# Kernel optimization log

Hardware: AMD Instinct MI355X
Metric: run time of the kernel (lower is better)

Reference implementation:

```python
import jax, jax.numpy as jnp
import numpy as np

B, T, X_DIM, H_DIM, C_NUM = 64, 1380, 96, 192, 345
SCALE = 1.0 / (X_DIM ** 0.5 * H_DIM ** 0.5)


def setup_inputs() -> dict:
    key = jax.random.key(0)
    k1, k2, k3, k4 = jax.random.split(key, 4)
    X = jax.random.normal(k1, (B, T, X_DIM), dtype=jnp.float32)
    H = jax.random.normal(k2, (B, T, H_DIM), dtype=jnp.float32)
    W1 = jax.random.normal(k3, (X_DIM, H_DIM), dtype=jnp.float32)
    W2 = jax.random.normal(k4, (C_NUM, T), dtype=jnp.float32)
    return {"X": X, "H": H, "W1": W1, "W2": W2}


def reference(X, H, W1, W2):
    # X: [B,T,x_dim] -> project to h_dim
    Xp = jnp.einsum('btx,xh->bth', X, W1)                 # [B,T,h]
    # batch_dot(X, H, axes=[2,2]) / sqrt(x_dim*h_dim)
    A = jnp.einsum('bth,buh->btu', Xp, H) * SCALE         # [B,T,T]
    # K.dot(W2, A) -> [c,B,T], then permute (1,0,2) -> [B,c,T]
    A = jnp.einsum('ct,btu->bcu', W2, A)                  # [B,c,T]
    A = jax.nn.softmax(A, axis=-1)
    # batch_dot(A, H, axes=[2,1])
    C = jnp.einsum('bcu,buh->bch', A, H)                  # [B,c,h]
    return C
```

## Files before the change

### kernel.cpp

```cpp
#include <hip/hip_runtime.h>
#include <math.h>

namespace {
constexpr int B_  = 64;
constexpr int T_  = 1380;
constexpr int XD_ = 96;
constexpr int HD_ = 192;
constexpr int CN_ = 345;
constexpr int CP_ = 384;
constexpr int TP_ = 1392;
constexpr int TP2_ = 1408;
constexpr int TH_ = 690;
constexpr float SCALE_ = 0.00736569563735987f;
}

typedef __attribute__((ext_vector_type(8))) short bf16x8;
typedef __attribute__((ext_vector_type(4))) float f32x4;
typedef unsigned short u16;
typedef unsigned int   u32;

__device__ __forceinline__ u16 f2bf(float f) {
    union { float f; u32 u; } c; c.f = f;
    u32 r = (c.u + 0x7fffu + ((c.u >> 16) & 1u)) >> 16;
    return (u16)r;
}
__device__ __forceinline__ float bf2f(u16 s) {
    union { u32 u; float f; } c; c.u = ((u32)s) << 16;
    return c.f;
}

__device__ __forceinline__ float red16_max(float v) {
    int ti;
    ti = __builtin_amdgcn_update_dpp(0, __builtin_bit_cast(int, v), 0x128, 0xf, 0xf, true);
    v = fmaxf(v, __builtin_bit_cast(float, ti));
    ti = __builtin_amdgcn_update_dpp(0, __builtin_bit_cast(int, v), 0x124, 0xf, 0xf, true);
    v = fmaxf(v, __builtin_bit_cast(float, ti));
    ti = __builtin_amdgcn_update_dpp(0, __builtin_bit_cast(int, v), 0x122, 0xf, 0xf, true);
    v = fmaxf(v, __builtin_bit_cast(float, ti));
    ti = __builtin_amdgcn_update_dpp(0, __builtin_bit_cast(int, v), 0x121, 0xf, 0xf, true);
    v = fmaxf(v, __builtin_bit_cast(float, ti));
    return v;
}
__device__ __forceinline__ float red16_sum(float v) {
    int ti;
    ti = __builtin_amdgcn_update_dpp(0, __builtin_bit_cast(int, v), 0x128, 0xf, 0xf, true);
    v += __builtin_bit_cast(float, ti);
    ti = __builtin_amdgcn_update_dpp(0, __builtin_bit_cast(int, v), 0x124, 0xf, 0xf, true);
    v += __builtin_bit_cast(float, ti);
    ti = __builtin_amdgcn_update_dpp(0, __builtin_bit_cast(int, v), 0x122, 0xf, 0xf, true);
    v += __builtin_bit_cast(float, ti);
    ti = __builtin_amdgcn_update_dpp(0, __builtin_bit_cast(int, v), 0x121, 0xf, 0xf, true);
    v += __builtin_bit_cast(float, ti);
    return v;
}

__global__ __launch_bounds__(256) void k0_all(const float* __restrict__ Hg,
                                              u16* __restrict__ Hh,
                                              u16* __restrict__ Hl,
                                              u16* __restrict__ Hth,
                                              const float* __restrict__ Xg,
                                              u16* __restrict__ Xth,
                                              u16* __restrict__ Xtl,
                                              const float* __restrict__ W2g,
                                              u16* __restrict__ W2h,
                                              u16* __restrict__ W2l,
                                              const float* __restrict__ W1g,
                                              u16* __restrict__ W1th,
                                              u16* __restrict__ W1tl) {
    __shared__ __align__(16) u16 sb[2][96][72];
    const int tid = threadIdx.x;
    const int L = blockIdx.x;

    if (L < 4224) {
        const int bx = L % 22, by = (L / 22) % 3, b = L / 66;
        const int u0 = bx * 64, h0 = by * 64;
        u16 (*til)[72] = sb[0];
#pragma unroll
        for (int i = 0; i < 2; i++) {
            int task = i * 256 + tid;
            int r = task >> 3;
            int g = task & 7;
            int u = u0 + r;
            float4 va = make_float4(0.f, 0.f, 0.f, 0.f), vb = va;
            if (u < T_) {
                const float* p = Hg + ((size_t)b * T_ + u) * HD_ + h0 + g * 8;
                va = *(const float4*)p;
                vb = *(const float4*)(p + 4);
            }
            float f[8] = {va.x, va.y, va.z, va.w, vb.x, vb.y, vb.z, vb.w};
            u16 hi[8], lo[8];
#pragma unroll
            for (int k = 0; k < 8; k++) {
                hi[k] = f2bf(f[k]);
                lo[k] = f2bf(f[k] - bf2f(hi[k]));
            }
            if (u < T_) {
                size_t base = ((size_t)b * T_ + u) * HD_ + h0 + g * 8;
                *(uint4*)(Hh + base) = *(const uint4*)hi;
                *(uint4*)(Hl + base) = *(const uint4*)lo;
            }
            const int rs = r ^ (g * 8);
#pragma unroll
            for (int k = 0; k < 8; k++) til[g * 8 + k][rs] = hi[k];
        }
        __syncthreads();
#pragma unroll
        for (int i = 0; i < 2; i++) {
            int task = i * 256 + tid;
            int hh = task >> 3;
            int ug = task & 7;
            int q  = ug ^ (hh >> 3);
            int ub = u0 + ug * 8;
            uint4 v = *(const uint4*)&til[hh][q * 8];
            u16* dst = Hth + ((size_t)b * HD_ + h0 + hh) * TP_ + ub;
            if (ub + 8 <= T_) {
                *(uint4*)dst = v;
            } else if (ub < TP_) {
                const u16* pv = (const u16*)&v;
#pragma unroll
                for (int k = 0; k < 8; k++)
                    if (ub + k < TP_) dst[k] = (ub + k < T_) ? pv[k] : (u16)0;
            }
        }
    } else if (L < 5632) {
        const int j = L - 4224;
        const int t0 = (j % 22) * 64, b = j / 22;
        u16 (*tih)[72] = sb[0];
        u16 (*tlo)[72] = sb[1];
#pragma unroll
        for (int i = 0; i < 6; i++) {
            int task = i * 256 + tid;
            int r = task / 24, xg = task % 24;
            float4 v = make_float4(0.f, 0.f, 0.f, 0.f);
            if (t0 + r < T_)
                v = *(const float4*)(Xg + ((size_t)b * T_ + t0 + r) * XD_ + xg * 4);
            float f[4] = {v.x, v.y, v.z, v.w};
            const int rs = r ^ (((xg >> 1) & 7) * 8);
#pragma unroll
            for (int k = 0; k < 4; k++) {
                u16 hi = f2bf(f[k]);
                tih[xg * 4 + k][rs] = hi;
                tlo[xg * 4 + k][rs] = f2bf(f[k] - bf2f(hi));
            }
        }
        __syncthreads();
#pragma unroll
        for (int i = 0; i < 6; i++) {
            int id = i * 256 + tid;
            int buf = (id >= 768);
            int cid = buf ? id - 768 : id;
            int x = cid >> 3, col = cid & 7;
            int q = col ^ ((x >> 3) & 7);
            uint4 v = *(const uint4*)&(buf ? tlo : tih)[x][q * 8];
            u16* dst = (buf ? Xtl : Xth) + ((size_t)b * XD_ + x) * TP2_ + t0 + col * 8;
            *(uint4*)dst = v;
        }
    } else {
        const int j = L - 5632;
        const int i = j * 256 + tid;
        const int n2 = CP_ * (TP2_ / 2);
        if (i < n2) {
            int c = i / (TP2_ / 2), tc = i % (TP2_ / 2);
            int t = tc * 2;
            float v0 = 0.f, v1 = 0.f;
            if (c < CN_) {
                if (t < T_)     v0 = W2g[(size_t)c * T_ + t];
                if (t + 1 < T_) v1 = W2g[(size_t)c * T_ + t + 1];
            }
            u16 h0 = f2bf(v0), h1 = f2bf(v1);
            u16 l0 = f2bf(v0 - bf2f(h0)), l1 = f2bf(v1 - bf2f(h1));
            ((u32*)W2h)[i] = (u32)h0 | ((u32)h1 << 16);
            ((u32*)W2l)[i] = (u32)l0 | ((u32)l1 << 16);
        } else {
            int i1 = i - n2;
            int h = i1 / XD_, x = i1 % XD_;
            float v = W1g[(size_t)x * HD_ + h];
            u16 hi = f2bf(v);
            W1th[i1] = hi;
            W1tl[i1] = f2bf(v - bf2f(hi));
        }
    }
}

__global__ __launch_bounds__(256, 1) void k12_mfma(const u16* __restrict__ W2h,
                                                   const u16* __restrict__ W2l,
                                                   const u16* __restrict__ Xth,
                                                   const u16* __restrict__ Xtl,
                                                   const u16* __restrict__ W1th,
                                                   const u16* __restrict__ W1tl,
                                                   u32* __restrict__ Ysi) {
    __shared__ __align__(16) u16 smem[49152];
    float* sZ = (float*)smem;

    const int tid  = threadIdx.x;
    const int lane = tid & 63;
    const int w    = tid >> 6;
    const int tx   = lane & 15;
    const int quad = lane >> 4;
    const int wr   = w >> 1;
    const int wc2  = w & 1;
    const int L    = blockIdx.x;
    const int xcd  = L & 7;
    const int slot = L >> 3;
    const int b    = xcd * 8 + (slot >> 2);
    const int c0   = (slot & 3) * 96;

    const u16* gsrc;
    size_t rowstart;
    if (w == 0)      { gsrc = W2h; rowstart = (size_t)c0; }
    else if (w == 1) { gsrc = W2l; rowstart = (size_t)c0; }
    else if (w == 2) { gsrc = Xth; rowstart = (size_t)b * XD_; }
    else             { gsrc = Xtl; rowstart = (size_t)b * XD_; }
    const int jg = (lane & 7) ^ ((lane >> 3) & 7);

#define STAGE(bufsel, kk)                                                         \
    {                                                                             \
        u16* lb = smem + (bufsel) * 24576 + w * 6144;                             \
        _Pragma("unroll")                                                         \
        for (int i_ = 0; i_ < 12; i_++) {                                         \
            int row_ = i_ * 8 + (lane >> 3);                                      \
            const u16* gp_ = gsrc + (rowstart + row_) * TP2_ + (kk) + jg * 8;     \
            __builtin_amdgcn_global_load_lds(                                     \
                (const __attribute__((address_space(1))) u32*)(const void*)gp_,   \
                (__attribute__((address_space(3))) u32*)(void*)(lb + i_ * 512),   \
                16, 0, 0);                                                        \
        }                                                                         \
    }

    f32x4 accZ[3][3];
#pragma unroll
    for (int i = 0; i < 3; i++)
#pragma unroll
        for (int j = 0; j < 3; j++) accZ[i][j] = (f32x4){0.f, 0.f, 0.f, 0.f};

    STAGE(0, 0);
    for (int s = 0; s < 22; s++) {
        __builtin_amdgcn_sched_barrier(0);
        if (s < 21) {
            STAGE((s + 1) & 1, (s + 1) * 64);
            asm volatile("s_waitcnt vmcnt(12)" ::: "memory");
        } else {
            asm volatile("s_waitcnt vmcnt(0)" ::: "memory");
        }
        __builtin_amdgcn_s_barrier();
        __builtin_amdgcn_sched_barrier(0);
        const u16* bufp = smem + (s & 1) * 24576;
#pragma unroll
        for (int ks2 = 0; ks2 < 2; ks2++) {
            const int G = ks2 * 4 + quad;
            bf16x8 ah[3], al[3], bh3[3], bl3[3];
#pragma unroll
            for (int am = 0; am < 3; am++) {
                int row = wr * 48 + am * 16 + tx;
                int off = row * 64 + (G ^ (row & 7)) * 8;
                ah[am] = *(const bf16x8*)(bufp + off);
                al[am] = *(const bf16x8*)(bufp + 6144 + off);
            }
#pragma unroll
            for (int bn = 0; bn < 3; bn++) {
                int row = wc2 * 48 + bn * 16 + tx;
                int off = row * 64 + (G ^ (row & 7)) * 8;
                bh3[bn] = *(const bf16x8*)(bufp + 12288 + off);
                bl3[bn] = *(const bf16x8*)(bufp + 18432 + off);
            }
#pragma unroll
            for (int am = 0; am < 3; am++)
#pragma unroll
                for (int bn = 0; bn < 3; bn++) {
                    accZ[am][bn] = __builtin_amdgcn_mfma_f32_16x16x32_bf16(ah[am], bh3[bn], accZ[am][bn], 0, 0, 0);
                    accZ[am][bn] = __builtin_amdgcn_mfma_f32_16x16x32_bf16(ah[am], bl3[bn], accZ[am][bn], 0, 0, 0);
                    accZ[am][bn] = __builtin_amdgcn_mfma_f32_16x16x32_bf16(al[am], bh3[bn], accZ[am][bn], 0, 0, 0);
                }
        }
        asm volatile("s_waitcnt lgkmcnt(0)" ::: "memory");
        __builtin_amdgcn_sched_barrier(0);
        __builtin_amdgcn_s_barrier();
    }
#undef STAGE

    __builtin_amdgcn_sched_barrier(0);
#pragma unroll
    for (int am = 0; am < 3; am++)
#pragma unroll
        for (int bn = 0; bn < 3; bn++)
#pragma unroll
            for (int r = 0; r < 4; r++)
                sZ[(wr * 48 + am * 16 + quad * 4 + r) * 100 + wc2 * 48 + bn * 16 + tx] = accZ[am][bn][r];
    __syncthreads();

    bf16x8 A2h[3][3], A2l[3][3];
#pragma unroll
    for (int am = 0; am < 3; am++)
#pragma unroll
        for (int ks = 0; ks < 3; ks++) {
            const float* zrow = sZ + (wr * 48 + am * 16 + tx) * 100 + ks * 32 + quad * 8;
            bf16x8 vh, vl;
#pragma unroll
            for (int j = 0; j < 8; j++) {
                float v = zrow[j];
                u16 hi = f2bf(v);
                vh[j] = (short)hi;
                vl[j] = (short)f2bf(v - bf2f(hi));
            }
            A2h[am][ks] = vh; A2l[am][ks] = vl;
        }

    f32x4 accY[3][6];
#pragma unroll
    for (int i = 0; i < 3; i++)
#pragma unroll
        for (int j = 0; j < 6; j++) accY[i][j] = (f32x4){0.f, 0.f, 0.f, 0.f};
#pragma unroll
    for (int hn = 0; hn < 6; hn++) {
        const int hrow = wc2 * 96 + hn * 16 + tx;
#pragma unroll
        for (int ks = 0; ks < 3; ks++) {
            bf16x8 bh = *(const bf16x8*)(W1th + (size_t)hrow * XD_ + ks * 32 + quad * 8);
            bf16x8 bl = *(const bf16x8*)(W1tl + (size_t)hrow * XD_ + ks * 32 + quad * 8);
#pragma unroll
            for (int am = 0; am < 3; am++) {
                accY[am][hn] = __builtin_amdgcn_mfma_f32_16x16x32_bf16(A2h[am][ks], bh, accY[am][hn], 0, 0, 0);
                accY[am][hn] = __builtin_amdgcn_mfma_f32_16x16x32_bf16(A2h[am][ks], bl, accY[am][hn], 0, 0, 0);
                accY[am][hn] = __builtin_amdgcn_mfma_f32_16x16x32_bf16(A2l[am][ks], bh, accY[am][hn], 0, 0, 0);
            }
        }
    }

#pragma unroll
    for (int am = 0; am < 3; am++)
#pragma unroll
        for (int r = 0; r < 4; r++) {
            int c = c0 + wr * 48 + am * 16 + quad * 4 + r;
            if (c < CN_) {
                size_t base = ((size_t)b * CN_ + c) * HD_;
#pragma unroll
                for (int hn = 0; hn < 6; hn++) {
                    float y = SCALE_ * accY[am][hn][r];
                    u16 hi = f2bf(y);
                    u16 lo = f2bf(y - bf2f(hi));
                    Ysi[base + wc2 * 96 + hn * 16 + tx] = (u32)hi | ((u32)lo << 16);
                }
            }
        }
}

__global__ __launch_bounds__(768, 3) void k3_mfma(const u32* __restrict__ Ysi,
                                                  const u16* __restrict__ Hh,
                                                  const u16* __restrict__ Hl,
                                                  const u16* __restrict__ Hth,
                                                  float* __restrict__ Op,
                                                  float* __restrict__ Ml,
                                                  float* __restrict__ Ll) {
    __shared__ __align__(16) u16 smem[44544];

    const int tid  = threadIdx.x;
    const int lane = tid & 63;
    const int w    = tid >> 6;
    const int tx   = lane & 15;
    const int quad = lane >> 4;
    const int L    = blockIdx.x;
    const int xcd  = L & 7;
    const int slot = L >> 3;
    const int gp   = xcd * 16 + (slot >> 1);
    const int ct   = slot & 1;
    const int b    = gp >> 1;
    const int sp   = gp & 1;
    const int c0   = ct * 192;
    const int us   = sp * TH_, ue = us + TH_;

    bf16x8 Ah[6], Al[6];
    const int ar = c0 + w * 16 + tx;
    if (ar < CN_) {
        const u32* yi = Ysi + ((size_t)b * CN_ + ar) * HD_;
#pragma unroll
        for (int ks = 0; ks < 6; ks++) {
            u32 vv[8];
            *(uint4*)&vv[0] = *(const uint4*)(yi + ks * 32 + quad * 8);
            *(uint4*)&vv[4] = *(const uint4*)(yi + ks * 32 + quad * 8 + 4);
            bf16x8 hh, ll;
#pragma unroll
            for (int j = 0; j < 8; j++) {
                hh[j] = (short)(vv[j] & 0xffffu);
                ll[j] = (short)(vv[j] >> 16);
            }
            Ah[ks] = hh; Al[ks] = ll;
        }
    } else {
#pragma unroll
        for (int ks = 0; ks < 6; ks++) { Ah[ks] = (bf16x8)0; Al[ks] = (bf16x8)0; }
    }

    float m_s[4], l_s[4];
    f32x4 accO[12];
#pragma unroll
    for (int r = 0; r < 4; r++) { m_s[r] = -1e30f; l_s[r] = 0.f; }
#pragma unroll
    for (int j = 0; j < 12; j++) accO[j] = (f32x4){0.f, 0.f, 0.f, 0.f};

    const char* srcp[3];
    u32 off0[3];
    const u32 incw = (u32)__builtin_amdgcn_readfirstlane((w < 8) ? (32 * HD_ * 2) : 64);
#pragma unroll
    for (int j = 0; j < 3; j++) {
        int k = w * 3 + j;
        u32 o;
        if (k < 24) {
            int arr = (k < 12) ? 0 : 1;
            int ii  = k - arr * 12;
            int cid = ii * 64 + lane;
            int u   = cid / 24, c1 = cid % 24;
            int c   = (c1 & ~7) | ((c1 & 7) ^ ((u >> 1) & 7));
            const u16* basep = (arr == 0 ? Hh : Hl) + (size_t)b * T_ * HD_;
            srcp[j] = (const char*)basep + ((size_t)(us + u) * HD_ + c * 8) * 2;
            o = (u32)(arr * 24576 + ii * 1024);
        } else {
            int ii  = k - 24;
            int cid = ii * 64 + lane;
            int h   = cid >> 2, c2 = cid & 3;
            int c   = c2 ^ ((h >> 2) & 3);
            const u16* basep = Hth + (size_t)b * HD_ * TP_;
            srcp[j] = (const char*)basep + ((size_t)h * TP_ + us + c * 8) * 2;
            o = (u32)(49152 + ii * 1024);
        }
        off0[j] = (u32)__builtin_amdgcn_readfirstlane((int)o);
    }

#define STAGE3(bufsel)                                                            \
    {                                                                             \
        _Pragma("unroll")                                                         \
        for (int j_ = 0; j_ < 3; j_++) {                                          \
            __builtin_amdgcn_global_load_lds(                                     \
                (const __attribute__((address_space(1))) u32*)(const void*)srcp[j_], \
                (__attribute__((address_space(3))) u32*)(void*)((char*)smem + off0[j_] + (bufsel) * 12288), \
                16, 0, 0);                                                        \
            srcp[j_] += incw;                                                     \
        }                                                                         \
    }

    u16* sPb = smem + 36864;

    STAGE3(0);
    for (int t = 0; t < 22; t++) {
        const int u0  = us + t * 32;
        const int buf = t & 1;
        __builtin_amdgcn_sched_barrier(0);
        if (t < 21) {
            STAGE3(buf ^ 1);
            asm volatile("s_waitcnt vmcnt(3)" ::: "memory");
        } else {
            asm volatile("s_waitcnt vmcnt(0)" ::: "memory");
        }
        __builtin_amdgcn_s_barrier();
        __builtin_amdgcn_sched_barrier(0);

        const u16* Hhb = smem + buf * 6144;
        const u16* Hlb = smem + 12288 + buf * 6144;
        const u16* Htb = smem + 24576 + buf * 6144;

        f32x4 s0a = {0.f, 0.f, 0.f, 0.f}, s1a = {0.f, 0.f, 0.f, 0.f};
        f32x4 s0b = {0.f, 0.f, 0.f, 0.f}, s1b = {0.f, 0.f, 0.f, 0.f};
        const int xr = (tx >> 1) & 7;
        __builtin_amdgcn_s_setprio(1);
#pragma unroll
        for (int ks = 0; ks < 6; ks++) {
            const int cc = ks * 4 + quad;
            const int cs = (cc & ~7) | ((cc & 7) ^ xr);
            const int ro0 = tx * 192 + cs * 8;
            const int ro1 = (16 + tx) * 192 + cs * 8;
            bf16x8 bh0 = *(const bf16x8*)(Hhb + ro0);
            bf16x8 bl0 = *(const bf16x8*)(Hlb + ro0);
            bf16x8 bh1 = *(const bf16x8*)(Hhb + ro1);
            bf16x8 bl1 = *(const bf16x8*)(Hlb + ro1);
            s0a = __builtin_amdgcn_mfma_f32_16x16x32_bf16(Ah[ks], bh0, s0a, 0, 0, 0);
            s1a = __builtin_amdgcn_mfma_f32_16x16x32_bf16(Ah[ks], bl0, s1a, 0, 0, 0);
            s1a = __builtin_amdgcn_mfma_f32_16x16x32_bf16(Al[ks], bh0, s1a, 0, 0, 0);
            s0b = __builtin_amdgcn_mfma_f32_16x16x32_bf16(Ah[ks], bh1, s0b, 0, 0, 0);
            s1b = __builtin_amdgcn_mfma_f32_16x16x32_bf16(Ah[ks], bl1, s1b, 0, 0, 0);
            s1b = __builtin_amdgcn_mfma_f32_16x16x32_bf16(Al[ks], bh1, s1b, 0, 0, 0);
        }
        __builtin_amdgcn_s_setprio(0);
        float sv0[4], sv1[4];
        const bool okA = (u0 + tx) < ue, okB = (u0 + 16 + tx) < ue;
#pragma unroll
        for (int r = 0; r < 4; r++) {
            sv0[r] = okA ? (s0a[r] + s1a[r]) : -1e30f;
            sv1[r] = okB ? (s0b[r] + s1b[r]) : -1e30f;
        }

        float alpha[4];
#pragma unroll
        for (int r = 0; r < 4; r++) {
            float mx = red16_max(fmaxf(sv0[r], sv1[r]));
            float mn = fmaxf(m_s[r], mx);
            alpha[r] = __expf(m_s[r] - mn);
            float p0 = __expf(sv0[r] - mn);
            float p1 = __expf(sv1[r] - mn);
            sPb[(w * 16 + quad * 4 + r) * 40 + tx]      = f2bf(p0);
            sPb[(w * 16 + quad * 4 + r) * 40 + 16 + tx] = f2bf(p1);
            float s = red16_sum(p0 + p1);
            l_s[r] = l_s[r] * alpha[r] + s;
            m_s[r] = mn;
        }
        f32x4 alv = {alpha[0], alpha[1], alpha[2], alpha[3]};
#pragma unroll
        for (int j = 0; j < 12; j++) accO[j] *= alv;

        bf16x8 pa = *(const bf16x8*)(sPb + (w * 16 + tx) * 40 + quad * 8);
        const int ctq = quad ^ ((tx >> 2) & 3);
        __builtin_amdgcn_s_setprio(1);
#pragma unroll
        for (int j = 0; j < 12; j++) {
            bf16x8 hb = *(const bf16x8*)(Htb + (j * 16 + tx) * 32 + ctq * 8);
            accO[j] = __builtin_amdgcn_mfma_f32_16x16x32_bf16(pa, hb, accO[j], 0, 0, 0);
        }
        __builtin_amdgcn_s_setprio(0);

        asm volatile("s_waitcnt lgkmcnt(0)" ::: "memory");
        __builtin_amdgcn_sched_barrier(0);
        __builtin_amdgcn_s_barrier();
    }
#undef STAGE3

#pragma unroll
    for (int r = 0; r < 4; r++) {
        int c = c0 + w * 16 + quad * 4 + r;
        if (c < CN_) {
            float* orow = Op + (((size_t)sp * B_ + b) * CN_ + c) * HD_;
#pragma unroll
            for (int j = 0; j < 12; j++) orow[j * 16 + tx] = accO[j][r];
            if (tx == 0) {
                size_t mi = ((size_t)sp * B_ + b) * CN_ + c;
                Ml[mi] = m_s[r];
                Ll[mi] = l_s[r];
            }
        }
    }
}

__global__ __launch_bounds__(256) void k_merge(const float* __restrict__ Op,
                                               const float* __restrict__ Ml,
                                               const float* __restrict__ Ll,
                                               float* __restrict__ out) {
    const int total = B_ * CN_ * (HD_ / 4);
    for (int i = blockIdx.x * 256 + threadIdx.x; i < total; i += gridDim.x * 256) {
        int f  = i % (HD_ / 4);
        int bc = i / (HD_ / 4);
        const size_t i0 = (size_t)bc;
        const size_t i1 = (size_t)B_ * CN_ + i0;
        float m0 = Ml[i0], m1 = Ml[i1];
        float l0 = Ll[i0], l1 = Ll[i1];
        float M  = fmaxf(m0, m1);
        float e0 = __expf(m0 - M), e1 = __expf(m1 - M);
        float inv = 1.0f / (l0 * e0 + l1 * e1);
        float4 o0 = *(const float4*)(Op + i0 * HD_ + f * 4);
        float4 o1 = *(const float4*)(Op + i1 * HD_ + f * 4);
        float4 r;
        r.x = (o0.x * e0 + o1.x * e1) * inv;
        r.y = (o0.y * e0 + o1.y * e1) * inv;
        r.z = (o0.z * e0 + o1.z * e1) * inv;
        r.w = (o0.w * e0 + o1.w * e1) * inv;
        *(float4*)(out + i0 * HD_ + f * 4) = r;
    }
}

extern "C" void kernel_launch(void* const* d_in, const int* in_sizes, int n_in,
                              void* d_out, int out_size, void* d_ws, size_t ws_size,
                              hipStream_t stream) {
    const float* X  = (const float*)d_in[0];
    const float* H  = (const float*)d_in[1];
    const float* W1 = (const float*)d_in[2];
    const float* W2 = (const float*)d_in[3];
    float* out = (float*)d_out;

    char* ws = (char*)d_ws;
    u32*   Ysi  = (u32*)(ws);
    u16*   Hh   = (u16*)(ws + 16957440);
    u16*   Hl   = (u16*)(ws + 50872320);
    u16*   Hth  = (u16*)(ws + 84787200);
    u16*   Xth  = (u16*)(ws + 118996992);
    u16*   Xtl  = (u16*)(ws + 136298496);
    float* Op   = (float*)(ws + 118996992);
    u16*   W2h  = (u16*)(ws + 153600000);
    u16*   W2l  = (u16*)(ws + 154681344);
    u16*   W1th = (u16*)(ws + 155762688);
    u16*   W1tl = (u16*)(ws + 155799552);
    float* Ml   = (float*)(ws + 155836416);
    float* Ll   = (float*)(ws + 156013056);

    k0_all  <<<dim3(6760),      256, 0, stream>>>(H, Hh, Hl, Hth,
                                                  X, Xth, Xtl,
                                                  W2, W2h, W2l,
                                                  W1, W1th, W1tl);
    k12_mfma<<<dim3(256),       256, 0, stream>>>(W2h, W2l, Xth, Xtl, W1th, W1tl, Ysi);
    k3_mfma <<<dim3(256),       768, 0, stream>>>(Ysi, Hh, Hl, Hth, Op, Ml, Ll);
    k_merge <<<dim3(2048),      256, 0, stream>>>(Op, Ml, Ll, out);
}
```

Baseline: 255.7 us.

## Fuse split-softmax merge into attention kernel via atomic last-block-done counter

Removes the separate merge kernel. Each k3 block writes its partial output, fences, and increments a per-(batch, c-tile) atomic counter that k0 zeroes. The second block to finish reads the other half's partial O/m/l and writes the merged normalized output directly from its registers. This saves one kernel launch and one full read/write pass over the partials, at the cost of a threadfence, an atomic per block, and a serialized tail in the last block.

```diff
diff --git a/kernel.cpp b/kernel.cpp
--- a/kernel.cpp
+++ b/kernel.cpp
@@ -66,7 +66,8 @@
                                               u16* __restrict__ W2l,
                                               const float* __restrict__ W1g,
                                               u16* __restrict__ W1th,
-                                              u16* __restrict__ W1tl) {
+                                              u16* __restrict__ W1tl,
+                                              u32* __restrict__ Tk) {
     __shared__ __align__(16) u16 sb[2][96][72];
     const int tid = threadIdx.x;
     const int L = blockIdx.x;
@@ -157,6 +158,7 @@
         }
     } else {
         const int j = L - 5632;
+        if (j == 0 && tid < 128) Tk[tid] = 0;
         const int i = j * 256 + tid;
         const int n2 = CP_ * (TP2_ / 2);
         if (i < n2) {
@@ -350,7 +352,9 @@
                                                   const u16* __restrict__ Hth,
                                                   float* __restrict__ Op,
                                                   float* __restrict__ Ml,
-                                                  float* __restrict__ Ll) {
+                                                  float* __restrict__ Ll,
+                                                  float* __restrict__ out,
+                                                  u32* __restrict__ Tk) {
     __shared__ __align__(16) u16 smem[44544];
 
     const int tid  = threadIdx.x;
@@ -535,31 +539,33 @@
             }
         }
     }
-}
-
-__global__ __launch_bounds__(256) void k_merge(const float* __restrict__ Op,
-                                               const float* __restrict__ Ml,
-                                               const float* __restrict__ Ll,
-                                               float* __restrict__ out) {
-    const int total = B_ * CN_ * (HD_ / 4);
-    for (int i = blockIdx.x * 256 + threadIdx.x; i < total; i += gridDim.x * 256) {
-        int f  = i % (HD_ / 4);
-        int bc = i / (HD_ / 4);
-        const size_t i0 = (size_t)bc;
-        const size_t i1 = (size_t)B_ * CN_ + i0;
-        float m0 = Ml[i0], m1 = Ml[i1];
-        float l0 = Ll[i0], l1 = Ll[i1];
-        float M  = fmaxf(m0, m1);
-        float e0 = __expf(m0 - M), e1 = __expf(m1 - M);
-        float inv = 1.0f / (l0 * e0 + l1 * e1);
-        float4 o0 = *(const float4*)(Op + i0 * HD_ + f * 4);
-        float4 o1 = *(const float4*)(Op + i1 * HD_ + f * 4);
-        float4 r;
-        r.x = (o0.x * e0 + o1.x * e1) * inv;
-        r.y = (o0.y * e0 + o1.y * e1) * inv;
-        r.z = (o0.z * e0 + o1.z * e1) * inv;
-        r.w = (o0.w * e0 + o1.w * e1) * inv;
-        *(float4*)(out + i0 * HD_ + f * 4) = r;
+
+    __threadfence();
+    __syncthreads();
+    if (tid == 0) ((u32*)smem)[0] = atomicAdd(&Tk[b * 2 + ct], 1u);
+    __syncthreads();
+    const u32 old = ((u32*)smem)[0];
+    if (old == 1) {
+        __threadfence();
+        const int spo = sp ^ 1;
+#pragma unroll
+        for (int r = 0; r < 4; r++) {
+            int c = c0 + w * 16 + quad * 4 + r;
+            if (c < CN_) {
+                size_t mio = ((size_t)spo * B_ + b) * CN_ + c;
+                float mo = Ml[mio], lo2 = Ll[mio];
+                float M  = fmaxf(m_s[r], mo);
+                float e0 = __expf(m_s[r] - M), e1 = __expf(mo - M);
+                float inv = 1.0f / (l_s[r] * e0 + lo2 * e1);
+                const float* oro = Op + mio * HD_;
+                float* dst = out + ((size_t)b * CN_ + c) * HD_;
+#pragma unroll
+                for (int j = 0; j < 12; j++) {
+                    float o1 = oro[j * 16 + tx];
+                    dst[j * 16 + tx] = (accO[j][r] * e0 + o1 * e1) * inv;
+                }
+            }
+        }
     }
 }
 
@@ -586,12 +592,12 @@
     u16*   W1tl = (u16*)(ws + 155799552);
     float* Ml   = (float*)(ws + 155836416);
     float* Ll   = (float*)(ws + 156013056);
+    u32*   Tk   = (u32*)(ws + 156189696);
 
     k0_all  <<<dim3(6760),      256, 0, stream>>>(H, Hh, Hl, Hth,
                                                   X, Xth, Xtl,
                                                   W2, W2h, W2l,
-                                                  W1, W1th, W1tl);
+                                                  W1, W1th, W1tl, Tk);
     k12_mfma<<<dim3(256),       256, 0, stream>>>(W2h, W2l, Xth, Xtl, W1th, W1tl, Ysi);
-    k3_mfma <<<dim3(256),       768, 0, stream>>>(Ysi, Hh, Hl, Hth, Op, Ml, Ll);
-    k_merge <<<dim3(2048),      256, 0, stream>>>(Op, Ml, Ll, out);
-}
+    k3_mfma <<<dim3(256),       768, 0, stream>>>(Ysi, Hh, Hl, Hth, Op, Ml, Ll, out, Tk);
+}
```

Result: slower. 386.0 us (+50.9%).
